# Kernel optimization log

Measured on AMD Instinct MI355X. Metric: run time of the kernel, lower is better.

Reference implementation:

```python
import jax, jax.numpy as jnp
import numpy as np

WINDOW_SIZE = 11
CHANNEL = 3
PAD = WINDOW_SIZE // 2
C1 = 0.01 ** 2
C2 = 0.03 ** 2
LEVEL_WEIGHTS = np.array([0.0448, 0.2856, 0.3001, 0.2363, 0.1333], dtype=np.float32)


def _make_window():
    # 1D Gaussian, sigma=1.5, normalized; outer product -> 2D window
    x = np.arange(WINDOW_SIZE, dtype=np.float32)
    g = np.exp(-((x - WINDOW_SIZE // 2) ** 2) / (2.0 * 1.5 ** 2))
    g = g / g.sum()
    w2 = np.outer(g, g).astype(np.float32)  # [11,11]
    # depthwise kernel [C, 1, 11, 11]
    return jnp.asarray(np.tile(w2[None, None], (CHANNEL, 1, 1, 1)))


def setup_inputs() -> dict:
    key = jax.random.key(0)
    k1, k2 = jax.random.split(key)
    img1 = jax.random.uniform(k1, (16, 3, 512, 512), dtype=jnp.float32)
    # correlated second image so cs stays positive (cs**weight well-defined)
    img2 = jnp.clip(img1 + 0.05 * jax.random.normal(k2, img1.shape, dtype=jnp.float32), 0.0, 1.0)
    return {"img1": img1, "img2": img2, "window": _make_window()}


def _dwconv(x, window):
    # depthwise 11x11 conv, SAME padding (pad=5), groups=C
    return jax.lax.conv_general_dilated(
        x, window, window_strides=(1, 1), padding=[(PAD, PAD), (PAD, PAD)],
        feature_group_count=CHANNEL,
        dimension_numbers=("NCHW", "OIHW", "NCHW"))


def _ssim_and_cs(img1, img2, window):
    mu1 = _dwconv(img1, window)
    mu2 = _dwconv(img2, window)
    mu1_sq = mu1 * mu1
    mu2_sq = mu2 * mu2
    mu1_mu2 = mu1 * mu2
    sigma1_sq = _dwconv(img1 * img1, window) - mu1_sq
    sigma2_sq = _dwconv(img2 * img2, window) - mu2_sq
    sigma12 = _dwconv(img1 * img2, window) - mu1_mu2
    cs_map = (2.0 * sigma12 + C2) / (sigma1_sq + sigma2_sq + C2)
    ssim_map = (2.0 * mu1_mu2 + C1) / (mu1_sq + mu2_sq + C1) * cs_map
    return jnp.mean(ssim_map), jnp.mean(cs_map)


def _avg_pool2(x):
    B, C, H, W = x.shape
    return x.reshape(B, C, H // 2, 2, W // 2, 2).mean(axis=(3, 5))


def reference(img1, img2, window):
    weights = jnp.asarray(LEVEL_WEIGHTS)
    levels = weights.shape[0]
    mssim, mcs = [], []
    for i in range(levels):
        s, c = _ssim_and_cs(img1, img2, window)
        mssim.append(s)
        mcs.append(c)
        if i < levels - 1:
            img1 = _avg_pool2(img1)
            img2 = _avg_pool2(img2)
    mssim = jnp.stack(mssim)
    mcs = jnp.stack(mcs)
    return jnp.prod(mcs[:-1] ** weights[:-1]) * mssim[-1] ** weights[-1]
```

## Files before the change

kernel.cpp:

```cpp
#include <hip/hip_runtime.h>
#include <math.h>

#define TW 16
#define THT 64
#define HRT 74
#define SS 66
#define HS 64
#define SC1 0.0001f
#define SC2 0.0009f
#define PLANES 48
#define NSLOT 64

typedef float v2f __attribute__((ext_vector_type(2)));

struct alignas(16) Smem {
    float sb[HRT * SS];
    float hb[HRT * HS];
    float rbuf[8];
};

template<bool GUARD>
__device__ __forceinline__ void ssim_tile(
        Smem* sm,
        const float* __restrict__ p1, const float* __restrict__ p2,
        int H, int W, int tx, int ty, int hrt, int level,
        const float* __restrict__ window,
        float* __restrict__ accum,
        float* __restrict__ l1a, float* __restrict__ l1b,
        float* __restrict__ l2a, float* __restrict__ l2b,
        float* __restrict__ l3a, float* __restrict__ l3b,
        float* __restrict__ l4a, float* __restrict__ l4b)
{
    const int tid = threadIdx.x;
    float* sb = sm->sb;
    float* hb = sm->hb;

    float g[11];
    {
        float invg5 = 1.0f / sqrtf(window[60]);
        #pragma unroll
        for (int k = 0; k < 11; ++k) g[k] = window[55 + k] * invg5;
    }

    const bool interior = (ty >= 5) && (ty + HRT - 6 < H) &&
                          (tx >= 8) && (tx + 24 <= W);
    if (interior) {
        for (int s = tid; s < HRT * 8; s += 256) {
            int r = s >> 3, j = s & 7;
            size_t o = (size_t)(ty + r - 5) * W + (tx - 8 + 4 * j);
            float4 a = *(const float4*)(p1 + o);
            float4 b = *(const float4*)(p2 + o);
            float* d = &sb[SS * r + 8 * j];
            *(float2*)(d)     = make_float2(a.x + b.x, a.x - b.x);
            *(float2*)(d + 2) = make_float2(a.y + b.y, a.y - b.y);
            *(float2*)(d + 4) = make_float2(a.z + b.z, a.z - b.z);
            *(float2*)(d + 6) = make_float2(a.w + b.w, a.w - b.w);
        }
    } else {
        for (int s = tid; s < hrt * 16; s += 256) {
            int r = s >> 4, j = s & 15;
            int gy = ty + r - 5;
            int gx = tx - 8 + 2 * j;
            float2 v1 = make_float2(0.f, 0.f), v2 = make_float2(0.f, 0.f);
            if ((unsigned)gy < (unsigned)H && (unsigned)gx < (unsigned)W) {
                size_t o = (size_t)gy * W + gx;
                v1 = *(const float2*)(p1 + o);
                v2 = *(const float2*)(p2 + o);
            }
            float* d = &sb[SS * r + 4 * j];
            *(float2*)(d)     = make_float2(v1.x + v2.x, v1.x - v2.x);
            *(float2*)(d + 2) = make_float2(v1.y + v2.y, v1.y - v2.y);
        }
    }
    __syncthreads();

    if (l1a) {
        int pc = tid & 7;
        int pr = tid >> 3;
        int r  = 2 * pr + 5;
        int x0 = 2 * (2 * pc + 8);
        const v2f* r0p = (const v2f*)&sb[SS * r + x0];
        const v2f* r1p = (const v2f*)&sb[SS * (r + 1) + x0];
        v2f s = (r0p[0] + r0p[1]) + (r1p[0] + r1p[1]);
        int W2 = W >> 1;
        size_t o = (size_t)((ty >> 1) + pr) * W2 + (tx >> 1) + pc;
        l1a[o] = 0.125f * (s.x + s.y);
        l1b[o] = 0.125f * (s.x - s.y);
    }

    if (l1a && tid >= 192) {
        const int lane = tid - 192;
        int qr = lane >> 2, qc = lane & 3;
        int rb = 4 * qr + 5, cb = 4 * qc + 8;
        v2f acc = {0.f, 0.f};
        #pragma unroll
        for (int i = 0; i < 4; ++i) {
            int ii = (i + qc) & 3;
            #pragma unroll
            for (int j = 0; j < 4; ++j) {
                int jr = (j + qr) & 3;
                acc += *(const v2f*)&sb[SS * (rb + ii) + 2 * (cb + jr)];
            }
        }
        float v2a = 0.03125f * (acc.x + acc.y), v2b = 0.03125f * (acc.x - acc.y);
        {
            int W4 = W >> 2;
            size_t o = (size_t)((ty >> 2) + qr) * W4 + (tx >> 2) + qc;
            l2a[o] = v2a;
            l2b[o] = v2b;
        }
        float v3a, v3b;
        {
            int tr = (lane >> 1) & 7, tc = lane & 1;
            int l00 = 8 * tr + 2 * tc;
            v3a = 0.25f * (__shfl(v2a, l00) + __shfl(v2a, l00 + 1) +
                           __shfl(v2a, l00 + 4) + __shfl(v2a, l00 + 5));
            v3b = 0.25f * (__shfl(v2b, l00) + __shfl(v2b, l00 + 1) +
                           __shfl(v2b, l00 + 4) + __shfl(v2b, l00 + 5));
            if (lane < 16) {
                int W8 = W >> 3;
                size_t o = (size_t)((ty >> 3) + tr) * W8 + (tx >> 3) + tc;
                l3a[o] = v3a;
                l3b[o] = v3b;
            }
        }
        {
            int ur = lane & 3;
            float v4a = 0.25f * (__shfl(v3a, 4 * ur) + __shfl(v3a, 4 * ur + 1) +
                                 __shfl(v3a, 4 * ur + 2) + __shfl(v3a, 4 * ur + 3));
            float v4b = 0.25f * (__shfl(v3b, 4 * ur) + __shfl(v3b, 4 * ur + 1) +
                                 __shfl(v3b, 4 * ur + 2) + __shfl(v3b, 4 * ur + 3));
            if (lane < 4) {
                int W16 = W >> 4;
                size_t o = (size_t)((ty >> 4) + ur) * W16 + (tx >> 4);
                l4a[o] = v4a;
                l4b[o] = v4b;
            }
        }
    }

    for (int gi = tid; gi < hrt * 4; gi += 256) {
        int r  = gi >> 2;
        int c0 = (gi & 3) << 2;
        const v2f* src = (const v2f*)&sb[SS * r + 2 * (c0 + 3)];
        v2f am[4] = {{0,0},{0,0},{0,0},{0,0}};
        v2f aq[4] = {{0,0},{0,0},{0,0},{0,0}};
        #pragma unroll
        for (int k = 0; k < 14; ++k) {
            v2f uv = src[k];
            v2f sq = uv * uv;
            #pragma unroll
            for (int q = 0; q < 4; ++q) {
                int t = k - q;
                if (t >= 0 && t < 11) {
                    v2f gg = {g[t], g[t]};
                    am[q] += gg * uv;
                    aq[q] += gg * sq;
                }
            }
        }
        int rx = (r & 1) << 2;
        #pragma unroll
        for (int q = 0; q < 4; ++q)
            *(float4*)&hb[HS * r + ((4 * (c0 + q)) ^ rx)] =
                make_float4(am[q].x, am[q].y, aq[q].x, aq[q].y);
    }
    __syncthreads();

    float ssum = 0.f, csum = 0.f;
    {
        int c  = tid & 15;
        int r0 = (tid >> 4) << 2;
        v2f M[4] = {{0,0},{0,0},{0,0},{0,0}};
        v2f Q[4] = {{0,0},{0,0},{0,0},{0,0}};
        #pragma unroll
        for (int k = 0; k < 14; ++k) {
            int R = r0 + k;
            float4 h = *(const float4*)&hb[HS * R + ((4 * c) ^ ((R & 1) << 2))];
            v2f hm = {h.x, h.y};
            v2f hq = {h.z, h.w};
            #pragma unroll
            for (int j = 0; j < 4; ++j) {
                int t = k - j;
                if (t >= 0 && t < 11) {
                    v2f gg = {g[t], g[t]};
                    M[j] += gg * hm;
                    Q[j] += gg * hq;
                }
            }
        }
        #pragma unroll
        for (int j = 0; j < 4; ++j) {
            if (!GUARD || (ty + r0 + j < H)) {
                float P = M[j].x * M[j].x, Qm = M[j].y * M[j].y;
                float A = 0.5f * (P - Qm);
                float B = 0.5f * (P + Qm);
                float su = 0.5f * (Q[j].x + Q[j].y);
                float sd = 0.5f * (Q[j].x - Q[j].y);
                float n1 = A + SC1;
                float d1 = B + SC1;
                float n2 = sd - A + SC2;
                float d2 = su - B + SC2;
                float inv = 1.f / (d1 * d2);
                csum += n2 * d1 * inv;
                ssum += n1 * n2 * inv;
            }
        }
    }

    #pragma unroll
    for (int off = 32; off; off >>= 1) {
        ssum += __shfl_down(ssum, off);
        csum += __shfl_down(csum, off);
    }
    const int wid = tid >> 6, lane = tid & 63;
    if (lane == 0) { sm->rbuf[wid * 2] = ssum; sm->rbuf[wid * 2 + 1] = csum; }
    __syncthreads();
    if (tid == 0) {
        float S = sm->rbuf[0] + sm->rbuf[2] + sm->rbuf[4] + sm->rbuf[6];
        float C = sm->rbuf[1] + sm->rbuf[3] + sm->rbuf[5] + sm->rbuf[7];
        int slot = (blockIdx.x + blockIdx.y * 7 + blockIdx.z * 13) & (NSLOT - 1);
        atomicAdd(&accum[(2 * level) * NSLOT + slot], S);
        atomicAdd(&accum[(2 * level + 1) * NSLOT + slot], C);
    }
}

__global__ __launch_bounds__(256, 4) void ssim_l0(
        const float* __restrict__ img1, const float* __restrict__ img2,
        const float* __restrict__ window, float* __restrict__ accum,
        float* __restrict__ l1a, float* __restrict__ l1b,
        float* __restrict__ l2a, float* __restrict__ l2b,
        float* __restrict__ l3a, float* __restrict__ l3b,
        float* __restrict__ l4a, float* __restrict__ l4b)
{
    __shared__ Smem sm;
    const int lin = blockIdx.x + (blockIdx.y << 5) + (blockIdx.z << 8);
    const int swz = (lin & 7) * 1536 + (lin >> 3);
    const int plane = swz >> 8;
    const int rem   = swz & 255;
    const int tyi   = rem >> 5;
    const int txi   = rem & 31;
    ssim_tile<false>(&sm,
              img1 + (size_t)plane * 512 * 512,
              img2 + (size_t)plane * 512 * 512,
              512, 512, txi * TW, tyi * THT, HRT, 0,
              window, accum,
              l1a + (size_t)plane * 256 * 256, l1b + (size_t)plane * 256 * 256,
              l2a + (size_t)plane * 128 * 128, l2b + (size_t)plane * 128 * 128,
              l3a + (size_t)plane * 64 * 64,   l3b + (size_t)plane * 64 * 64,
              l4a + (size_t)plane * 32 * 32,   l4b + (size_t)plane * 32 * 32);
}

__global__ __launch_bounds__(256, 4) void ssim_l1(
        const float* __restrict__ l1a, const float* __restrict__ l1b,
        const float* __restrict__ window, float* __restrict__ accum)
{
    __shared__ Smem sm;
    const int lin = blockIdx.x + (blockIdx.z << 6);
    const int swz = (lin & 7) * 384 + (lin >> 3);
    const int plane = swz >> 6;
    const int rem   = swz & 63;
    const int tiy   = rem >> 4;
    const int tix   = rem & 15;
    const float* p1 = l1a + (size_t)plane * 256 * 256;
    const float* p2 = l1b + (size_t)plane * 256 * 256;
    ssim_tile<false>(&sm, p1, p2, 256, 256, tix * TW, tiy * THT, HRT, 1,
              window, accum,
              nullptr, nullptr, nullptr, nullptr,
              nullptr, nullptr, nullptr, nullptr);
}

__global__ __launch_bounds__(256, 4) void ssim_l234(
        const float* __restrict__ l2a, const float* __restrict__ l2b,
        const float* __restrict__ l3a, const float* __restrict__ l3b,
        const float* __restrict__ l4a, const float* __restrict__ l4b,
        const float* __restrict__ window, float* __restrict__ accum)
{
    __shared__ Smem sm;
    const int x = blockIdx.x;
    const int plane = blockIdx.z;
    int level, H, tix, tiy;
    const float *b1, *b2;
    if (x < 16)      { level = 2; H = 128; tix = x & 7;  tiy = x >> 3; b1 = l2a; b2 = l2b; }
    else if (x < 20) { level = 3; H = 64;  tix = x - 16; tiy = 0;      b1 = l3a; b2 = l3b; }
    else             { level = 4; H = 32;  tix = x - 20; tiy = 0;      b1 = l4a; b2 = l4b; }
    const float* p1 = b1 + (size_t)plane * H * H;
    const float* p2 = b2 + (size_t)plane * H * H;
    int ty = tiy * THT;
    int hrt = min(HRT, H - ty + 10);
    ssim_tile<true>(&sm, p1, p2, H, H, tix * TW, ty, hrt, level,
              window, accum,
              nullptr, nullptr, nullptr, nullptr,
              nullptr, nullptr, nullptr, nullptr);
}

__global__ void finalize_kernel(const float* __restrict__ accum, float* __restrict__ out) {
    int t = threadIdx.x;
    float sums[10];
    #pragma unroll
    for (int i = 0; i < 10; ++i) {
        float v = accum[i * NSLOT + t];
        #pragma unroll
        for (int off = 32; off; off >>= 1) v += __shfl_down(v, off);
        sums[i] = v;
    }
    if (t == 0) {
        const float w[5] = {0.0448f, 0.2856f, 0.3001f, 0.2363f, 0.1333f};
        float res = 1.f;
        #pragma unroll
        for (int L = 0; L < 4; ++L) {
            float dim = (float)(512 >> L);
            float cnt = (float)PLANES * dim * dim;
            res *= powf(sums[2 * L + 1] / cnt, w[L]);
        }
        float cnt4 = (float)PLANES * 32.f * 32.f;
        res *= powf(sums[8] / cnt4, w[4]);
        out[0] = res;
    }
}

extern "C" void kernel_launch(void* const* d_in, const int* in_sizes, int n_in,
                              void* d_out, int out_size, void* d_ws, size_t ws_size,
                              hipStream_t stream) {
    const float* img1   = (const float*)d_in[0];
    const float* img2   = (const float*)d_in[1];
    const float* window = (const float*)d_in[2];
    float* out = (float*)d_out;
    float* ws  = (float*)d_ws;

    float* accum = ws;
    const size_t S1 = (size_t)PLANES * 256 * 256;
    const size_t S2 = (size_t)PLANES * 128 * 128;
    const size_t S3 = (size_t)PLANES * 64 * 64;
    const size_t S4 = (size_t)PLANES * 32 * 32;
    float* l1a = ws + 1024;    float* l1b = l1a + S1;
    float* l2a = l1b + S1;     float* l2b = l2a + S2;
    float* l3a = l2b + S2;     float* l3b = l3a + S3;
    float* l4a = l3b + S3;     float* l4b = l4a + S4;

    hipMemsetAsync(accum, 0, 10 * NSLOT * sizeof(float), stream);

    ssim_l0<<<dim3(512 / TW, 512 / THT, PLANES), 256, 0, stream>>>(
        img1, img2, window, accum,
        l1a, l1b, l2a, l2b, l3a, l3b, l4a, l4b);

    ssim_l1<<<dim3(64, 1, PLANES), 256, 0, stream>>>(l1a, l1b, window, accum);

    ssim_l234<<<dim3(22, 1, PLANES), 256, 0, stream>>>(
        l2a, l2b, l3a, l3b, l4a, l4b, window, accum);

    finalize_kernel<<<1, 64, 0, stream>>>(accum, out);
}
```

Baseline: 223.9 us.

## Store pyramid levels as interleaved u/v pairs and merge later-level kernels with finalize

Pyramid levels 1-4 are now written as interleaved (sum, difference) float2 pairs, so the later levels load them straight into shared memory without recomputing sum and difference. The level-1 kernel, the level-2-4 kernel and the finalize kernel are merged into one launch. The last block to finish, detected with an atomic counter, performs the final reduction. This removes two kernel launches and their tail gaps. It costs a serialized last-block reduction and requires the counter to be zeroed by the widened memset.

```diff
diff --git a/kernel.cpp b/kernel.cpp
--- a/kernel.cpp
+++ b/kernel.cpp
@@ -10,6 +10,7 @@
 #define SC2 0.0009f
 #define PLANES 48
 #define NSLOT 64
+#define REST_BLOCKS (86 * PLANES)
 
 typedef float v2f __attribute__((ext_vector_type(2)));
 
@@ -19,17 +20,17 @@
     float rbuf[8];
 };
 
-template<bool GUARD>
+template<bool UVIN, bool GUARD>
 __device__ __forceinline__ void ssim_tile(
         Smem* sm,
         const float* __restrict__ p1, const float* __restrict__ p2,
         int H, int W, int tx, int ty, int hrt, int level,
         const float* __restrict__ window,
         float* __restrict__ accum,
-        float* __restrict__ l1a, float* __restrict__ l1b,
-        float* __restrict__ l2a, float* __restrict__ l2b,
-        float* __restrict__ l3a, float* __restrict__ l3b,
-        float* __restrict__ l4a, float* __restrict__ l4b)
+        float* __restrict__ l1uv,
+        float* __restrict__ l2uv,
+        float* __restrict__ l3uv,
+        float* __restrict__ l4uv)
 {
     const int tid = threadIdx.x;
     float* sb = sm->sb;
@@ -44,37 +45,61 @@
 
     const bool interior = (ty >= 5) && (ty + HRT - 6 < H) &&
                           (tx >= 8) && (tx + 24 <= W);
-    if (interior) {
-        for (int s = tid; s < HRT * 8; s += 256) {
-            int r = s >> 3, j = s & 7;
-            size_t o = (size_t)(ty + r - 5) * W + (tx - 8 + 4 * j);
-            float4 a = *(const float4*)(p1 + o);
-            float4 b = *(const float4*)(p2 + o);
-            float* d = &sb[SS * r + 8 * j];
-            *(float2*)(d)     = make_float2(a.x + b.x, a.x - b.x);
-            *(float2*)(d + 2) = make_float2(a.y + b.y, a.y - b.y);
-            *(float2*)(d + 4) = make_float2(a.z + b.z, a.z - b.z);
-            *(float2*)(d + 6) = make_float2(a.w + b.w, a.w - b.w);
+    if (!UVIN) {
+        if (interior) {
+            for (int s = tid; s < HRT * 8; s += 256) {
+                int r = s >> 3, j = s & 7;
+                size_t o = (size_t)(ty + r - 5) * W + (tx - 8 + 4 * j);
+                float4 a = *(const float4*)(p1 + o);
+                float4 b = *(const float4*)(p2 + o);
+                float* d = &sb[SS * r + 8 * j];
+                *(float2*)(d)     = make_float2(a.x + b.x, a.x - b.x);
+                *(float2*)(d + 2) = make_float2(a.y + b.y, a.y - b.y);
+                *(float2*)(d + 4) = make_float2(a.z + b.z, a.z - b.z);
+                *(float2*)(d + 6) = make_float2(a.w + b.w, a.w - b.w);
+            }
+        } else {
+            for (int s = tid; s < hrt * 16; s += 256) {
+                int r = s >> 4, j = s & 15;
+                int gy = ty + r - 5;
+                int gx = tx - 8 + 2 * j;
+                float2 v1 = make_float2(0.f, 0.f), v2 = make_float2(0.f, 0.f);
+                if ((unsigned)gy < (unsigned)H && (unsigned)gx < (unsigned)W) {
+                    size_t o = (size_t)gy * W + gx;
+                    v1 = *(const float2*)(p1 + o);
+                    v2 = *(const float2*)(p2 + o);
+                }
+                float* d = &sb[SS * r + 4 * j];
+                *(float2*)(d)     = make_float2(v1.x + v2.x, v1.x - v2.x);
+                *(float2*)(d + 2) = make_float2(v1.y + v2.y, v1.y - v2.y);
+            }
         }
     } else {
-        for (int s = tid; s < hrt * 16; s += 256) {
-            int r = s >> 4, j = s & 15;
-            int gy = ty + r - 5;
-            int gx = tx - 8 + 2 * j;
-            float2 v1 = make_float2(0.f, 0.f), v2 = make_float2(0.f, 0.f);
-            if ((unsigned)gy < (unsigned)H && (unsigned)gx < (unsigned)W) {
-                size_t o = (size_t)gy * W + gx;
-                v1 = *(const float2*)(p1 + o);
-                v2 = *(const float2*)(p2 + o);
-            }
-            float* d = &sb[SS * r + 4 * j];
-            *(float2*)(d)     = make_float2(v1.x + v2.x, v1.x - v2.x);
-            *(float2*)(d + 2) = make_float2(v1.y + v2.y, v1.y - v2.y);
+        if (interior) {
+            for (int s = tid; s < HRT * 8; s += 256) {
+                int r = s >> 3, j = s & 7;
+                const float* src = p1 + ((size_t)(ty + r - 5) * W + (tx - 8 + 4 * j)) * 2;
+                float4 A = *(const float4*)(src);
+                float4 B = *(const float4*)(src + 4);
+                float* d = &sb[SS * r + 8 * j];
+                *(float4*)(d)     = A;
+                *(float4*)(d + 4) = B;
+            }
+        } else {
+            for (int s = tid; s < hrt * 16; s += 256) {
+                int r = s >> 4, j = s & 15;
+                int gy = ty + r - 5;
+                int gx = tx - 8 + 2 * j;
+                float4 v = make_float4(0.f, 0.f, 0.f, 0.f);
+                if ((unsigned)gy < (unsigned)H && (unsigned)gx < (unsigned)W)
+                    v = *(const float4*)(p1 + ((size_t)gy * W + gx) * 2);
+                *(float4*)&sb[SS * r + 4 * j] = v;
+            }
         }
     }
     __syncthreads();
 
-    if (l1a) {
+    if (l1uv) {
         int pc = tid & 7;
         int pr = tid >> 3;
         int r  = 2 * pr + 5;
@@ -83,12 +108,11 @@
         const v2f* r1p = (const v2f*)&sb[SS * (r + 1) + x0];
         v2f s = (r0p[0] + r0p[1]) + (r1p[0] + r1p[1]);
         int W2 = W >> 1;
-        size_t o = (size_t)((ty >> 1) + pr) * W2 + (tx >> 1) + pc;
-        l1a[o] = 0.125f * (s.x + s.y);
-        l1b[o] = 0.125f * (s.x - s.y);
-    }
-
-    if (l1a && tid >= 192) {
+        size_t o = ((size_t)((ty >> 1) + pr) * W2 + (tx >> 1) + pc) * 2;
+        *(float2*)(l1uv + o) = make_float2(0.25f * s.x, 0.25f * s.y);
+    }
+
+    if (l1uv && tid >= 192) {
         const int lane = tid - 192;
         int qr = lane >> 2, qc = lane & 3;
         int rb = 4 * qr + 5, cb = 4 * qc + 8;
@@ -102,39 +126,36 @@
                 acc += *(const v2f*)&sb[SS * (rb + ii) + 2 * (cb + jr)];
             }
         }
-        float v2a = 0.03125f * (acc.x + acc.y), v2b = 0.03125f * (acc.x - acc.y);
+        float u2 = 0.0625f * acc.x, v2 = 0.0625f * acc.y;
         {
             int W4 = W >> 2;
-            size_t o = (size_t)((ty >> 2) + qr) * W4 + (tx >> 2) + qc;
-            l2a[o] = v2a;
-            l2b[o] = v2b;
-        }
-        float v3a, v3b;
+            size_t o = ((size_t)((ty >> 2) + qr) * W4 + (tx >> 2) + qc) * 2;
+            *(float2*)(l2uv + o) = make_float2(u2, v2);
+        }
+        float u3, v3;
         {
             int tr = (lane >> 1) & 7, tc = lane & 1;
             int l00 = 8 * tr + 2 * tc;
-            v3a = 0.25f * (__shfl(v2a, l00) + __shfl(v2a, l00 + 1) +
-                           __shfl(v2a, l00 + 4) + __shfl(v2a, l00 + 5));
-            v3b = 0.25f * (__shfl(v2b, l00) + __shfl(v2b, l00 + 1) +
-                           __shfl(v2b, l00 + 4) + __shfl(v2b, l00 + 5));
+            u3 = 0.25f * (__shfl(u2, l00) + __shfl(u2, l00 + 1) +
+                          __shfl(u2, l00 + 4) + __shfl(u2, l00 + 5));
+            v3 = 0.25f * (__shfl(v2, l00) + __shfl(v2, l00 + 1) +
+                          __shfl(v2, l00 + 4) + __shfl(v2, l00 + 5));
             if (lane < 16) {
                 int W8 = W >> 3;
-                size_t o = (size_t)((ty >> 3) + tr) * W8 + (tx >> 3) + tc;
-                l3a[o] = v3a;
-                l3b[o] = v3b;
+                size_t o = ((size_t)((ty >> 3) + tr) * W8 + (tx >> 3) + tc) * 2;
+                *(float2*)(l3uv + o) = make_float2(u3, v3);
             }
         }
         {
             int ur = lane & 3;
-            float v4a = 0.25f * (__shfl(v3a, 4 * ur) + __shfl(v3a, 4 * ur + 1) +
-                                 __shfl(v3a, 4 * ur + 2) + __shfl(v3a, 4 * ur + 3));
-            float v4b = 0.25f * (__shfl(v3b, 4 * ur) + __shfl(v3b, 4 * ur + 1) +
-                                 __shfl(v3b, 4 * ur + 2) + __shfl(v3b, 4 * ur + 3));
+            float u4 = 0.25f * (__shfl(u3, 4 * ur) + __shfl(u3, 4 * ur + 1) +
+                                __shfl(u3, 4 * ur + 2) + __shfl(u3, 4 * ur + 3));
+            float v4 = 0.25f * (__shfl(v3, 4 * ur) + __shfl(v3, 4 * ur + 1) +
+                                __shfl(v3, 4 * ur + 2) + __shfl(v3, 4 * ur + 3));
             if (lane < 4) {
                 int W16 = W >> 4;
-                size_t o = (size_t)((ty >> 4) + ur) * W16 + (tx >> 4);
-                l4a[o] = v4a;
-                l4b[o] = v4b;
+                size_t o = ((size_t)((ty >> 4) + ur) * W16 + (tx >> 4)) * 2;
+                *(float2*)(l4uv + o) = make_float2(u4, v4);
             }
         }
     }
@@ -228,10 +249,8 @@
 __global__ __launch_bounds__(256, 4) void ssim_l0(
         const float* __restrict__ img1, const float* __restrict__ img2,
         const float* __restrict__ window, float* __restrict__ accum,
-        float* __restrict__ l1a, float* __restrict__ l1b,
-        float* __restrict__ l2a, float* __restrict__ l2b,
-        float* __restrict__ l3a, float* __restrict__ l3b,
-        float* __restrict__ l4a, float* __restrict__ l4b)
+        float* __restrict__ l1uv, float* __restrict__ l2uv,
+        float* __restrict__ l3uv, float* __restrict__ l4uv)
 {
     __shared__ Smem sm;
     const int lin = blockIdx.x + (blockIdx.y << 5) + (blockIdx.z << 8);
@@ -240,82 +259,68 @@
     const int rem   = swz & 255;
     const int tyi   = rem >> 5;
     const int txi   = rem & 31;
-    ssim_tile<false>(&sm,
+    ssim_tile<false, false>(&sm,
               img1 + (size_t)plane * 512 * 512,
               img2 + (size_t)plane * 512 * 512,
               512, 512, txi * TW, tyi * THT, HRT, 0,
               window, accum,
-              l1a + (size_t)plane * 256 * 256, l1b + (size_t)plane * 256 * 256,
-              l2a + (size_t)plane * 128 * 128, l2b + (size_t)plane * 128 * 128,
-              l3a + (size_t)plane * 64 * 64,   l3b + (size_t)plane * 64 * 64,
-              l4a + (size_t)plane * 32 * 32,   l4b + (size_t)plane * 32 * 32);
+              l1uv + (size_t)plane * 256 * 256 * 2,
+              l2uv + (size_t)plane * 128 * 128 * 2,
+              l3uv + (size_t)plane * 64 * 64 * 2,
+              l4uv + (size_t)plane * 32 * 32 * 2);
 }
 
-__global__ __launch_bounds__(256, 4) void ssim_l1(
-        const float* __restrict__ l1a, const float* __restrict__ l1b,
-        const float* __restrict__ window, float* __restrict__ accum)
-{
-    __shared__ Smem sm;
-    const int lin = blockIdx.x + (blockIdx.z << 6);
-    const int swz = (lin & 7) * 384 + (lin >> 3);
-    const int plane = swz >> 6;
-    const int rem   = swz & 63;
-    const int tiy   = rem >> 4;
-    const int tix   = rem & 15;
-    const float* p1 = l1a + (size_t)plane * 256 * 256;
-    const float* p2 = l1b + (size_t)plane * 256 * 256;
-    ssim_tile<false>(&sm, p1, p2, 256, 256, tix * TW, tiy * THT, HRT, 1,
-              window, accum,
-              nullptr, nullptr, nullptr, nullptr,
-              nullptr, nullptr, nullptr, nullptr);
-}
-
-__global__ __launch_bounds__(256, 4) void ssim_l234(
-        const float* __restrict__ l2a, const float* __restrict__ l2b,
-        const float* __restrict__ l3a, const float* __restrict__ l3b,
-        const float* __restrict__ l4a, const float* __restrict__ l4b,
-        const float* __restrict__ window, float* __restrict__ accum)
+__global__ __launch_bounds__(256, 4) void ssim_rest(
+        const float* __restrict__ l1uv, const float* __restrict__ l2uv,
+        const float* __restrict__ l3uv, const float* __restrict__ l4uv,
+        const float* __restrict__ window, float* __restrict__ accum,
+        unsigned int* __restrict__ cnt, float* __restrict__ out)
 {
     __shared__ Smem sm;
     const int x = blockIdx.x;
     const int plane = blockIdx.z;
     int level, H, tix, tiy;
-    const float *b1, *b2;
-    if (x < 16)      { level = 2; H = 128; tix = x & 7;  tiy = x >> 3; b1 = l2a; b2 = l2b; }
-    else if (x < 20) { level = 3; H = 64;  tix = x - 16; tiy = 0;      b1 = l3a; b2 = l3b; }
-    else             { level = 4; H = 32;  tix = x - 20; tiy = 0;      b1 = l4a; b2 = l4b; }
-    const float* p1 = b1 + (size_t)plane * H * H;
-    const float* p2 = b2 + (size_t)plane * H * H;
+    const float *b;
+    if (x < 64)      { level = 1; H = 256; tix = x & 15;           tiy = x >> 4;      b = l1uv; }
+    else if (x < 80) { level = 2; H = 128; int i = x - 64; tix = i & 7; tiy = i >> 3; b = l2uv; }
+    else if (x < 84) { level = 3; H = 64;  int i = x - 80; tix = i;     tiy = 0;      b = l3uv; }
+    else             { level = 4; H = 32;  int i = x - 84; tix = i;     tiy = 0;      b = l4uv; }
+    const float* p = b + (size_t)plane * H * H * 2;
     int ty = tiy * THT;
     int hrt = min(HRT, H - ty + 10);
-    ssim_tile<true>(&sm, p1, p2, H, H, tix * TW, ty, hrt, level,
-              window, accum,
-              nullptr, nullptr, nullptr, nullptr,
-              nullptr, nullptr, nullptr, nullptr);
-}
-
-__global__ void finalize_kernel(const float* __restrict__ accum, float* __restrict__ out) {
-    int t = threadIdx.x;
-    float sums[10];
-    #pragma unroll
-    for (int i = 0; i < 10; ++i) {
-        float v = accum[i * NSLOT + t];
-        #pragma unroll
-        for (int off = 32; off; off >>= 1) v += __shfl_down(v, off);
-        sums[i] = v;
-    }
-    if (t == 0) {
-        const float w[5] = {0.0448f, 0.2856f, 0.3001f, 0.2363f, 0.1333f};
-        float res = 1.f;
-        #pragma unroll
-        for (int L = 0; L < 4; ++L) {
-            float dim = (float)(512 >> L);
-            float cnt = (float)PLANES * dim * dim;
-            res *= powf(sums[2 * L + 1] / cnt, w[L]);
-        }
-        float cnt4 = (float)PLANES * 32.f * 32.f;
-        res *= powf(sums[8] / cnt4, w[4]);
-        out[0] = res;
+    ssim_tile<true, true>(&sm, p, p, H, H, tix * TW, ty, hrt, level,
+              window, accum, nullptr, nullptr, nullptr, nullptr);
+
+    const int tid = threadIdx.x;
+    if (tid == 0) {
+        __threadfence();
+        unsigned old = atomicAdd(cnt, 1u);
+        sm.rbuf[0] = (old == REST_BLOCKS - 1) ? 1.f : 0.f;
+    }
+    __syncthreads();
+    if (sm.rbuf[0] != 0.f && tid < 64) {
+        __threadfence();
+        float sums[10];
+        #pragma unroll
+        for (int i = 0; i < 10; ++i) {
+            float v = atomicAdd(&accum[i * NSLOT + tid], 0.0f);
+            #pragma unroll
+            for (int off = 32; off; off >>= 1) v += __shfl_down(v, off);
+            sums[i] = v;
+        }
+        if (tid == 0) {
+            const float w[5] = {0.0448f, 0.2856f, 0.3001f, 0.2363f, 0.1333f};
+            float res = 1.f;
+            #pragma unroll
+            for (int L = 0; L < 4; ++L) {
+                float dim = (float)(512 >> L);
+                float cntf = (float)PLANES * dim * dim;
+                res *= powf(sums[2 * L + 1] / cntf, w[L]);
+            }
+            float cnt4 = (float)PLANES * 32.f * 32.f;
+            res *= powf(sums[8] / cnt4, w[4]);
+            out[0] = res;
+        }
     }
 }
 
@@ -329,25 +334,20 @@
     float* ws  = (float*)d_ws;
 
     float* accum = ws;
+    unsigned int* cnt = (unsigned int*)(ws + 1008);
     const size_t S1 = (size_t)PLANES * 256 * 256;
     const size_t S2 = (size_t)PLANES * 128 * 128;
     const size_t S3 = (size_t)PLANES * 64 * 64;
-    const size_t S4 = (size_t)PLANES * 32 * 32;
-    float* l1a = ws + 1024;    float* l1b = l1a + S1;
-    float* l2a = l1b + S1;     float* l2b = l2a + S2;
-    float* l3a = l2b + S2;     float* l3b = l3a + S3;
-    float* l4a = l3b + S3;     float* l4b = l4a + S4;
-
-    hipMemsetAsync(accum, 0, 10 * NSLOT * sizeof(float), stream);
+    float* l1uv = ws + 1024;
+    float* l2uv = l1uv + 2 * S1;
+    float* l3uv = l2uv + 2 * S2;
+    float* l4uv = l3uv + 2 * S3;
+
+    hipMemsetAsync(ws, 0, 4096, stream);
 
     ssim_l0<<<dim3(512 / TW, 512 / THT, PLANES), 256, 0, stream>>>(
-        img1, img2, window, accum,
-        l1a, l1b, l2a, l2b, l3a, l3b, l4a, l4b);
-
-    ssim_l1<<<dim3(64, 1, PLANES), 256, 0, stream>>>(l1a, l1b, window, accum);
-
-    ssim_l234<<<dim3(22, 1, PLANES), 256, 0, stream>>>(
-        l2a, l2b, l3a, l3b, l4a, l4b, window, accum);
-
-    finalize_kernel<<<1, 64, 0, stream>>>(accum, out);
+        img1, img2, window, accum, l1uv, l2uv, l3uv, l4uv);
+
+    ssim_rest<<<dim3(86, 1, PLANES), 256, 0, stream>>>(
+        l1uv, l2uv, l3uv, l4uv, window, accum, cnt, out);
 }
```

Result: slower. 292.4 us (+30.6%).
